# Optimization experiments

Measured on AMD Instinct MI355X. Metric: run time of the kernel, lower is better.

Reference implementation:

```python
import jax, jax.numpy as jnp
import numpy as np

MIN_FOCAL = 50.0
MIN_DISTANCE = 0.25
Z_EPS = 1e-4
V, N = 64, 500000


def _euler_xyz_to_matrix(euler):
    # euler: [V,3] -> R = Rx @ Ry @ Rz : [V,3,3]
    c = jnp.cos(euler); s = jnp.sin(euler)
    cx, cy, cz = c[:, 0], c[:, 1], c[:, 2]
    sx, sy, sz = s[:, 0], s[:, 1], s[:, 2]
    one = jnp.ones_like(cx); zero = jnp.zeros_like(cx)
    rx = jnp.stack([
        jnp.stack([one, zero, zero], -1),
        jnp.stack([zero, cx, -sx], -1),
        jnp.stack([zero, sx, cx], -1)], -2)
    ry = jnp.stack([
        jnp.stack([cy, zero, sy], -1),
        jnp.stack([zero, one, zero], -1),
        jnp.stack([-sy, zero, cy], -1)], -2)
    rz = jnp.stack([
        jnp.stack([cz, -sz, zero], -1),
        jnp.stack([sz, cz, zero], -1),
        jnp.stack([zero, zero, one], -1)], -2)
    return rx @ ry @ rz


def setup_inputs() -> dict:
    key = jax.random.key(0)
    k1, k2, k3, k4, k5 = jax.random.split(key, 5)
    points = jax.random.normal(k1, (N, 3), dtype=jnp.float32) * 2.0
    euler = jax.random.normal(k2, (V, 3), dtype=jnp.float32) * 0.2
    translation_xy = jax.random.normal(k3, (V, 2), dtype=jnp.float32) * 0.1
    translation_depth_raw = jax.random.normal(k4, (V,), dtype=jnp.float32)
    focal_raw = jax.random.uniform(k5, (1,), dtype=jnp.float32) * 5.0 + 5.0
    return {
        'points': points,
        'euler': euler,
        'translation_xy': translation_xy,
        'translation_depth_raw': translation_depth_raw,
        'focal_raw': focal_raw,
        'cx': 640,
        'cy': 360,
    }


def reference(points, euler, translation_xy, translation_depth_raw, focal_raw, cx, cy):
    rotations = _euler_xyz_to_matrix(euler)                       # [V,3,3]
    cam = jnp.einsum('vij,nj->vni', rotations, points)            # [V,N,3]
    depth = jax.nn.softplus(translation_depth_raw) + MIN_DISTANCE  # [V]
    translations = jnp.concatenate([translation_xy, -depth[:, None]], axis=-1)  # [V,3]
    cam = cam + translations[:, None, :]
    z = cam[..., 2]
    z_sign = jnp.where(z >= 0, 1.0, -1.0)
    safe_z = z_sign * jnp.maximum(jnp.abs(z), Z_EPS)
    focal = jax.nn.softplus(focal_raw[0]) + MIN_FOCAL
    u = -focal * cam[..., 0] / safe_z + cx
    v = focal * cam[..., 1] / safe_z + cy
    return jnp.stack([u, v], axis=-1)                              # [V,N,2]
```

## Files before the change

### kernel.cpp

```cpp
#include <hip/hip_runtime.h>
#include <math.h>


#define NVIEW 64
#define BLOCK 256
#define PPT 2
#define Z_EPS 1e-4f

__device__ __forceinline__ float softplus_f(float x) {
    return fmaxf(x, 0.0f) + log1pf(expf(-fabsf(x)));
}

__global__ __launch_bounds__(BLOCK) void ba_project_kernel(
    const float* __restrict__ points,
    const float* __restrict__ euler,
    const float* __restrict__ txy,
    const float* __restrict__ tdr,
    const float* __restrict__ focal_raw,
    const int*   __restrict__ cxp,
    const int*   __restrict__ cyp,
    float2* __restrict__ out,
    int N)
{
    __shared__ float4 vd[NVIEW * 3];

    const int tid = threadIdx.x;

    if (tid < NVIEW) {
        float ex = euler[tid * 3 + 0];
        float ey = euler[tid * 3 + 1];
        float ez = euler[tid * 3 + 2];
        float sx, cx_, sy, cy_, sz, cz;
        sincosf(ex, &sx, &cx_);
        sincosf(ey, &sy, &cy_);
        sincosf(ez, &sz, &cz);
        float r00 = cy_ * cz;
        float r01 = -cy_ * sz;
        float r02 = sy;
        float r10 = cx_ * sz + sx * sy * cz;
        float r11 = cx_ * cz - sx * sy * sz;
        float r12 = -sx * cy_;
        float r20 = sx * sz - cx_ * sy * cz;
        float r21 = sx * cz + cx_ * sy * sz;
        float r22 = cx_ * cy_;

        float tx = txy[tid * 2 + 0];
        float ty = txy[tid * 2 + 1];
        float tz = -(softplus_f(tdr[tid]) + 0.25f);

        vd[tid * 3 + 0] = make_float4(r00, r01, r02, tx);
        vd[tid * 3 + 1] = make_float4(r10, r11, r12, ty);
        vd[tid * 3 + 2] = make_float4(r20, r21, r22, tz);
    }
    __syncthreads();

    const float focal = softplus_f(focal_raw[0]) + 50.0f;
    const float ccx = (float)cxp[0];
    const float ccy = (float)cyp[0];

    const int base = blockIdx.x * (BLOCK * PPT) + tid;

    float px[PPT], py[PPT], pz[PPT];
    int   n[PPT];
    bool  ok[PPT];
#pragma unroll
    for (int k = 0; k < PPT; ++k) {
        n[k]  = base + k * BLOCK;
        ok[k] = n[k] < N;
        int i = ok[k] ? n[k] * 3 : 0;
        px[k] = points[i + 0];
        py[k] = points[i + 1];
        pz[k] = points[i + 2];
    }

    for (int v = 0; v < NVIEW; ++v) {
        float4 ra = vd[v * 3 + 0];
        float4 rb = vd[v * 3 + 1];
        float4 rc = vd[v * 3 + 2];
#pragma unroll
        for (int k = 0; k < PPT; ++k) {
            float X = fmaf(ra.x, px[k], fmaf(ra.y, py[k], fmaf(ra.z, pz[k], ra.w)));
            float Y = fmaf(rb.x, px[k], fmaf(rb.y, py[k], fmaf(rb.z, pz[k], rb.w)));
            float Z = fmaf(rc.x, px[k], fmaf(rc.y, py[k], fmaf(rc.z, pz[k], rc.w)));

            float sgn  = (Z >= 0.0f) ? 1.0f : -1.0f;
            float safe = sgn * fmaxf(fabsf(Z), Z_EPS);

            float t = focal * __builtin_amdgcn_rcpf(safe);

            float u = fmaf(-X, t, ccx);
            float w = fmaf( Y, t, ccy);

            if (ok[k]) out[(size_t)v * N + n[k]] = make_float2(u, w);
        }
    }
}

extern "C" void kernel_launch(void* const* d_in, const int* in_sizes, int n_in,
                              void* d_out, int out_size, void* d_ws, size_t ws_size,
                              hipStream_t stream) {
    const float* points    = (const float*)d_in[0];
    const float* euler     = (const float*)d_in[1];
    const float* txy       = (const float*)d_in[2];
    const float* tdr       = (const float*)d_in[3];
    const float* focal_raw = (const float*)d_in[4];
    const int*   cxp       = (const int*)d_in[5];
    const int*   cyp       = (const int*)d_in[6];

    const int N = in_sizes[0] / 3;
    const int blocks = (N + BLOCK * PPT - 1) / (BLOCK * PPT);

    ba_project_kernel<<<blocks, BLOCK, 0, stream>>>(
        points, euler, txy, tdr, focal_raw, cxp, cyp, (float2*)d_out, N);
}
```

Measured before the change: 260.5 us.

## Split views across grid.y and write adjacent point pairs with 16-byte stores

Each thread now handles two adjacent points, loaded as three float2 reads and written per view as a single float4 store instead of two strided float2 stores. The 64 views are split into groups of 16 across a second grid dimension, which gives more blocks and shorter per-thread loops. The focal length and the sign of u are folded into the shared rotation rows, which removes a multiply per projection. Point loads are repeated once per view group, and the float4 stores assume N is even (or a matching offset) to stay 16-byte aligned.

```diff
diff --git a/kernel.cpp b/kernel.cpp
--- a/kernel.cpp
+++ b/kernel.cpp
@@ -3,8 +3,8 @@
 
 
 #define NVIEW 64
+#define VT 16
 #define BLOCK 256
-#define PPT 2
 #define Z_EPS 1e-4f
 
 __device__ __forceinline__ float softplus_f(float x) {
@@ -22,14 +22,16 @@
     float2* __restrict__ out,
     int N)
 {
-    __shared__ float4 vd[NVIEW * 3];
+    __shared__ float4 vd[VT * 3];
 
     const int tid = threadIdx.x;
+    const float focal = softplus_f(focal_raw[0]) + 50.0f;
 
-    if (tid < NVIEW) {
-        float ex = euler[tid * 3 + 0];
-        float ey = euler[tid * 3 + 1];
-        float ez = euler[tid * 3 + 2];
+    if (tid < VT) {
+        const int v = blockIdx.y * VT + tid;
+        float ex = euler[v * 3 + 0];
+        float ey = euler[v * 3 + 1];
+        float ez = euler[v * 3 + 2];
         float sx, cx_, sy, cy_, sz, cz;
         sincosf(ex, &sx, &cx_);
         sincosf(ey, &sy, &cy_);
@@ -44,55 +46,67 @@
         float r21 = sx * cz + cx_ * sy * sz;
         float r22 = cx_ * cy_;
 
-        float tx = txy[tid * 2 + 0];
-        float ty = txy[tid * 2 + 1];
-        float tz = -(softplus_f(tdr[tid]) + 0.25f);
+        float tx = txy[v * 2 + 0];
+        float ty = txy[v * 2 + 1];
+        float tz = -(softplus_f(tdr[v]) + 0.25f);
 
-        vd[tid * 3 + 0] = make_float4(r00, r01, r02, tx);
-        vd[tid * 3 + 1] = make_float4(r10, r11, r12, ty);
+        vd[tid * 3 + 0] = make_float4(-focal * r00, -focal * r01, -focal * r02, -focal * tx);
+        vd[tid * 3 + 1] = make_float4( focal * r10,  focal * r11,  focal * r12,  focal * ty);
         vd[tid * 3 + 2] = make_float4(r20, r21, r22, tz);
     }
     __syncthreads();
 
-    const float focal = softplus_f(focal_raw[0]) + 50.0f;
     const float ccx = (float)cxp[0];
     const float ccy = (float)cyp[0];
 
-    const int base = blockIdx.x * (BLOCK * PPT) + tid;
+    const int pair = blockIdx.x * BLOCK + tid;
+    const int n0 = pair * 2;
+    if (n0 >= N) return;
+    const bool full = (n0 + 1 < N);
 
-    float px[PPT], py[PPT], pz[PPT];
-    int   n[PPT];
-    bool  ok[PPT];
-#pragma unroll
-    for (int k = 0; k < PPT; ++k) {
-        n[k]  = base + k * BLOCK;
-        ok[k] = n[k] < N;
-        int i = ok[k] ? n[k] * 3 : 0;
-        px[k] = points[i + 0];
-        py[k] = points[i + 1];
-        pz[k] = points[i + 2];
+    const float2* p2 = (const float2*)points;
+    float2 a = p2[pair * 3 + 0];
+    float2 b, c;
+    if (full) {
+        b = p2[pair * 3 + 1];
+        c = p2[pair * 3 + 2];
+    } else {
+        b = make_float2(points[(size_t)n0 * 3 + 2], 0.0f);
+        c = make_float2(0.0f, 0.0f);
     }
+    const float x0 = a.x, y0 = a.y, z0 = b.x;
+    const float x1 = b.y, y1 = c.x, z1 = c.y;
 
-    for (int v = 0; v < NVIEW; ++v) {
-        float4 ra = vd[v * 3 + 0];
-        float4 rb = vd[v * 3 + 1];
-        float4 rc = vd[v * 3 + 2];
-#pragma unroll
-        for (int k = 0; k < PPT; ++k) {
-            float X = fmaf(ra.x, px[k], fmaf(ra.y, py[k], fmaf(ra.z, pz[k], ra.w)));
-            float Y = fmaf(rb.x, px[k], fmaf(rb.y, py[k], fmaf(rb.z, pz[k], rb.w)));
-            float Z = fmaf(rc.x, px[k], fmaf(rc.y, py[k], fmaf(rc.z, pz[k], rc.w)));
+    float2* outp = out + (size_t)(blockIdx.y * VT) * N + n0;
 
-            float sgn  = (Z >= 0.0f) ? 1.0f : -1.0f;
-            float safe = sgn * fmaxf(fabsf(Z), Z_EPS);
+#pragma unroll 2
+    for (int v = 0; v < VT; ++v) {
+        float4 A = vd[v * 3 + 0];
+        float4 B = vd[v * 3 + 1];
+        float4 C = vd[v * 3 + 2];
 
-            float t = focal * __builtin_amdgcn_rcpf(safe);
+        float X0 = fmaf(A.x, x0, fmaf(A.y, y0, fmaf(A.z, z0, A.w)));
+        float Y0 = fmaf(B.x, x0, fmaf(B.y, y0, fmaf(B.z, z0, B.w)));
+        float Z0 = fmaf(C.x, x0, fmaf(C.y, y0, fmaf(C.z, z0, C.w)));
+        float sg0  = (Z0 >= 0.0f) ? 1.0f : -1.0f;
+        float t0   = __builtin_amdgcn_rcpf(sg0 * fmaxf(fabsf(Z0), Z_EPS));
+        float u0 = fmaf(X0, t0, ccx);
+        float w0 = fmaf(Y0, t0, ccy);
 
-            float u = fmaf(-X, t, ccx);
-            float w = fmaf( Y, t, ccy);
+        float X1 = fmaf(A.x, x1, fmaf(A.y, y1, fmaf(A.z, z1, A.w)));
+        float Y1 = fmaf(B.x, x1, fmaf(B.y, y1, fmaf(B.z, z1, B.w)));
+        float Z1 = fmaf(C.x, x1, fmaf(C.y, y1, fmaf(C.z, z1, C.w)));
+        float sg1  = (Z1 >= 0.0f) ? 1.0f : -1.0f;
+        float t1   = __builtin_amdgcn_rcpf(sg1 * fmaxf(fabsf(Z1), Z_EPS));
+        float u1 = fmaf(X1, t1, ccx);
+        float w1 = fmaf(Y1, t1, ccy);
 
-            if (ok[k]) out[(size_t)v * N + n[k]] = make_float2(u, w);
+        if (full) {
+            *(float4*)outp = make_float4(u0, w0, u1, w1);
+        } else {
+            *outp = make_float2(u0, w0);
         }
+        outp += N;
     }
 }
 
@@ -108,8 +122,9 @@
     const int*   cyp       = (const int*)d_in[6];
 
     const int N = in_sizes[0] / 3;
-    const int blocks = (N + BLOCK * PPT - 1) / (BLOCK * PPT);
+    const int pairs = (N + 1) / 2;
+    dim3 grid((pairs + BLOCK - 1) / BLOCK, NVIEW / VT, 1);
 
-    ba_project_kernel<<<blocks, BLOCK, 0, stream>>>(
+    ba_project_kernel<<<grid, dim3(BLOCK, 1, 1), 0, stream>>>(
         points, euler, txy, tdr, focal_raw, cxp, cyp, (float2*)d_out, N);
 }
```

Result: slower. 277.2 us (+6.4%).

## Parallelize over views in grid with vectorized loads and nontemporal wide stores

Applied to the files above, without the earlier changes.

Moves the view loop into the grid's x dimension so each block computes one view's rotation in registers, removing the shared-memory table and barrier. Each thread now handles eight contiguous points, loading them with float4 reads and writing results with 16-byte nontemporal stores. Focal is folded into the rotation rows to save multiplies. The trade-off is that points are re-read once per view, relying on cache, and the sincos setup is repeated in every block.

```diff
diff --git a/kernel.cpp b/kernel.cpp
--- a/kernel.cpp
+++ b/kernel.cpp
@@ -4,8 +4,10 @@
 
 #define NVIEW 64
 #define BLOCK 256
-#define PPT 2
+#define PPT 8
 #define Z_EPS 1e-4f
+
+typedef float floatx4 __attribute__((ext_vector_type(4)));
 
 __device__ __forceinline__ float softplus_f(float x) {
     return fmaxf(x, 0.0f) + log1pf(expf(-fabsf(x)));
@@ -22,76 +24,84 @@
     float2* __restrict__ out,
     int N)
 {
-    __shared__ float4 vd[NVIEW * 3];
-
-    const int tid = threadIdx.x;
-
-    if (tid < NVIEW) {
-        float ex = euler[tid * 3 + 0];
-        float ey = euler[tid * 3 + 1];
-        float ez = euler[tid * 3 + 2];
-        float sx, cx_, sy, cy_, sz, cz;
-        sincosf(ex, &sx, &cx_);
-        sincosf(ey, &sy, &cy_);
-        sincosf(ez, &sz, &cz);
-        float r00 = cy_ * cz;
-        float r01 = -cy_ * sz;
-        float r02 = sy;
-        float r10 = cx_ * sz + sx * sy * cz;
-        float r11 = cx_ * cz - sx * sy * sz;
-        float r12 = -sx * cy_;
-        float r20 = sx * sz - cx_ * sy * cz;
-        float r21 = sx * cz + cx_ * sy * sz;
-        float r22 = cx_ * cy_;
-
-        float tx = txy[tid * 2 + 0];
-        float ty = txy[tid * 2 + 1];
-        float tz = -(softplus_f(tdr[tid]) + 0.25f);
-
-        vd[tid * 3 + 0] = make_float4(r00, r01, r02, tx);
-        vd[tid * 3 + 1] = make_float4(r10, r11, r12, ty);
-        vd[tid * 3 + 2] = make_float4(r20, r21, r22, tz);
-    }
-    __syncthreads();
+    const int v = blockIdx.x;
 
     const float focal = softplus_f(focal_raw[0]) + 50.0f;
+
+    float ex = euler[v * 3 + 0];
+    float ey = euler[v * 3 + 1];
+    float ez = euler[v * 3 + 2];
+    float sx, cx_, sy, cy_, sz, cz;
+    sincosf(ex, &sx, &cx_);
+    sincosf(ey, &sy, &cy_);
+    sincosf(ez, &sz, &cz);
+    float r00 = cy_ * cz;
+    float r01 = -cy_ * sz;
+    float r02 = sy;
+    float r10 = cx_ * sz + sx * sy * cz;
+    float r11 = cx_ * cz - sx * sy * sz;
+    float r12 = -sx * cy_;
+    float r20 = sx * sz - cx_ * sy * cz;
+    float r21 = sx * cz + cx_ * sy * sz;
+    float r22 = cx_ * cy_;
+
+    float tx = txy[v * 2 + 0];
+    float ty = txy[v * 2 + 1];
+    float tz = -(softplus_f(tdr[v]) + 0.25f);
+
+    const float a0 = -focal * r00, a1 = -focal * r01, a2 = -focal * r02, a3 = -focal * tx;
+    const float b0 =  focal * r10, b1 =  focal * r11, b2 =  focal * r12, b3 =  focal * ty;
     const float ccx = (float)cxp[0];
     const float ccy = (float)cyp[0];
 
-    const int base = blockIdx.x * (BLOCK * PPT) + tid;
+    const int n0 = (blockIdx.y * BLOCK + threadIdx.x) * PPT;
+    if (n0 >= N) return;
 
-    float px[PPT], py[PPT], pz[PPT];
-    int   n[PPT];
-    bool  ok[PPT];
-#pragma unroll
-    for (int k = 0; k < PPT; ++k) {
-        n[k]  = base + k * BLOCK;
-        ok[k] = n[k] < N;
-        int i = ok[k] ? n[k] * 3 : 0;
-        px[k] = points[i + 0];
-        py[k] = points[i + 1];
-        pz[k] = points[i + 2];
-    }
+    float2* orow = out + (size_t)v * N + n0;
 
-    for (int v = 0; v < NVIEW; ++v) {
-        float4 ra = vd[v * 3 + 0];
-        float4 rb = vd[v * 3 + 1];
-        float4 rc = vd[v * 3 + 2];
+    if (n0 + PPT <= N) {
+        const float4* src = (const float4*)(points + (size_t)n0 * 3);
+        float4 L0 = src[0], L1 = src[1], L2 = src[2];
+        float4 L3 = src[3], L4 = src[4], L5 = src[5];
+        const float P[PPT][3] = {
+            {L0.x, L0.y, L0.z}, {L0.w, L1.x, L1.y},
+            {L1.z, L1.w, L2.x}, {L2.y, L2.z, L2.w},
+            {L3.x, L3.y, L3.z}, {L3.w, L4.x, L4.y},
+            {L4.z, L4.w, L5.x}, {L5.y, L5.z, L5.w}};
+
+        float uv[PPT * 2];
 #pragma unroll
         for (int k = 0; k < PPT; ++k) {
-            float X = fmaf(ra.x, px[k], fmaf(ra.y, py[k], fmaf(ra.z, pz[k], ra.w)));
-            float Y = fmaf(rb.x, px[k], fmaf(rb.y, py[k], fmaf(rb.z, pz[k], rb.w)));
-            float Z = fmaf(rc.x, px[k], fmaf(rc.y, py[k], fmaf(rc.z, pz[k], rc.w)));
+            float X = fmaf(a0, P[k][0], fmaf(a1, P[k][1], fmaf(a2, P[k][2], a3)));
+            float Y = fmaf(b0, P[k][0], fmaf(b1, P[k][1], fmaf(b2, P[k][2], b3)));
+            float Z = fmaf(r20, P[k][0], fmaf(r21, P[k][1], fmaf(r22, P[k][2], tz)));
+            float sg = (Z >= 0.0f) ? 1.0f : -1.0f;
+            float t  = __builtin_amdgcn_rcpf(sg * fmaxf(fabsf(Z), Z_EPS));
+            uv[k * 2 + 0] = fmaf(X, t, ccx);
+            uv[k * 2 + 1] = fmaf(Y, t, ccy);
+        }
 
-            float sgn  = (Z >= 0.0f) ? 1.0f : -1.0f;
-            float safe = sgn * fmaxf(fabsf(Z), Z_EPS);
-
-            float t = focal * __builtin_amdgcn_rcpf(safe);
-
-            float u = fmaf(-X, t, ccx);
-            float w = fmaf( Y, t, ccy);
-
-            if (ok[k]) out[(size_t)v * N + n[k]] = make_float2(u, w);
+        floatx4* o4 = (floatx4*)orow;
+#pragma unroll
+        for (int k = 0; k < PPT / 2; ++k) {
+            floatx4 val;
+            val.x = uv[4 * k + 0];
+            val.y = uv[4 * k + 1];
+            val.z = uv[4 * k + 2];
+            val.w = uv[4 * k + 3];
+            __builtin_nontemporal_store(val, &o4[k]);
+        }
+    } else {
+        for (int k = 0; k < PPT && n0 + k < N; ++k) {
+            float x = points[(size_t)(n0 + k) * 3 + 0];
+            float y = points[(size_t)(n0 + k) * 3 + 1];
+            float z = points[(size_t)(n0 + k) * 3 + 2];
+            float X = fmaf(a0, x, fmaf(a1, y, fmaf(a2, z, a3)));
+            float Y = fmaf(b0, x, fmaf(b1, y, fmaf(b2, z, b3)));
+            float Z = fmaf(r20, x, fmaf(r21, y, fmaf(r22, z, tz)));
+            float sg = (Z >= 0.0f) ? 1.0f : -1.0f;
+            float t  = __builtin_amdgcn_rcpf(sg * fmaxf(fabsf(Z), Z_EPS));
+            orow[k] = make_float2(fmaf(X, t, ccx), fmaf(Y, t, ccy));
         }
     }
 }
@@ -108,8 +118,10 @@
     const int*   cyp       = (const int*)d_in[6];
 
     const int N = in_sizes[0] / 3;
-    const int blocks = (N + BLOCK * PPT - 1) / (BLOCK * PPT);
+    const int chunk = BLOCK * PPT;
+    const int nchunks = (N + chunk - 1) / chunk;
+    dim3 grid(NVIEW, nchunks, 1);
 
-    ba_project_kernel<<<blocks, BLOCK, 0, stream>>>(
+    ba_project_kernel<<<grid, dim3(BLOCK, 1, 1), 0, stream>>>(
         points, euler, txy, tdr, focal_raw, cxp, cyp, (float2*)d_out, N);
 }
```

After: 600.2 us. 130% more time.
